# Kernel tuning notes

Measured on AMD Instinct MI355X. Metric: run time of the kernel, lower is better.

## Reference

```python
import jax, jax.numpy as jnp
import numpy as np

B, S, D, H = 4, 2048, 1024, 16
DH = D // H


def _rope_tables():
    # standard RoPE angle tables, shaped [1, S, 1, DH] as the module expects
    inv_freq = 1.0 / (10000.0 ** (np.arange(0, DH, 2, dtype=np.float32) / DH))
    ang = np.arange(S, dtype=np.float32)[:, None] * inv_freq[None, :]  # [S, DH/2]
    ang = np.concatenate([ang, ang], axis=-1)  # [S, DH]
    cos = jnp.asarray(np.cos(ang))[None, :, None, :]
    sin = jnp.asarray(np.sin(ang))[None, :, None, :]
    return cos, sin


def setup_inputs() -> dict:
    key = jax.random.key(0)
    ks = jax.random.split(key, 5)
    x = jax.random.normal(ks[0], (B, S, D), dtype=jnp.float32)
    wq = jax.random.normal(ks[1], (D, D), dtype=jnp.float32) * 0.02
    wk = jax.random.normal(ks[2], (D, D), dtype=jnp.float32) * 0.02
    wv = jax.random.normal(ks[3], (D, D), dtype=jnp.float32) * 0.02
    wo = jax.random.normal(ks[4], (D, D), dtype=jnp.float32) * 0.02
    cos, sin = _rope_tables()
    return {"x": x, "cos": cos, "sin": sin, "wq": wq, "wk": wk, "wv": wv, "wo": wo}


def _rotate_half(t):
    t1, t2 = t[..., : DH // 2], t[..., DH // 2:]
    return jnp.concatenate([-t2, t1], axis=-1)


def reference(x, cos, sin, wq, wk, wv, wo):
    b, s, d = x.shape
    # QKV projections (torch Linear: y = x @ W.T), reshape to [B, H, S, DH]
    q = (x @ wq.T).reshape(b, s, H, DH).transpose(0, 2, 1, 3)
    k = (x @ wk.T).reshape(b, s, H, DH).transpose(0, 2, 1, 3)
    v = (x @ wv.T).reshape(b, s, H, DH).transpose(0, 2, 1, 3)
    # permute(0,2,1,3): [1,S,1,DH] -> [1,1,S,DH]; slice [:, :s] is a no-op on the size-1 head dim
    cos_p = jnp.transpose(cos, (0, 2, 1, 3))[:, :s]
    sin_p = jnp.transpose(sin, (0, 2, 1, 3))[:, :s]
    q = q * cos_p + _rotate_half(q) * sin_p
    k = k * cos_p + _rotate_half(k) * sin_p
    # SDPA (no mask, dropout_p = 0)
    scores = jnp.einsum("bhqd,bhkd->bhqk", q, k) / jnp.sqrt(jnp.float32(DH))
    attn = jax.nn.softmax(scores, axis=-1)
    out = jnp.einsum("bhqk,bhkd->bhqd", attn, v)
    out = out.transpose(0, 2, 1, 3).reshape(b, s, d)
    return out @ wo.T
```

## Files before the change

kernel.cpp:

```cpp
#include <hip/hip_runtime.h>
#include <hip/hip_bf16.h>
#include <stdint.h>

#define B 4
#define S 2048
#define D 1024
#define H 16
#define DH 64
#define M_TOT (B*S)
#define BH (B*H)

typedef unsigned short u16;
typedef unsigned int u32;
typedef __attribute__((ext_vector_type(4))) float f32x4;
typedef __attribute__((ext_vector_type(16))) float f32x16;
typedef __attribute__((ext_vector_type(8))) short bf16x8;
typedef __attribute__((ext_vector_type(2))) unsigned int u32x2;

typedef const __attribute__((address_space(1))) unsigned int* gp_t;
typedef __attribute__((address_space(3))) unsigned int* lp_t;

__device__ __forceinline__ void gload_lds16(const void* g, void* l) {
    __builtin_amdgcn_global_load_lds((gp_t)g, (lp_t)l, 16, 0, 0);
}

__device__ __forceinline__ float bf2f(u16 u) {
    u32 t = ((u32)u) << 16;
    float f; __builtin_memcpy(&f, &t, 4); return f;
}
__device__ __forceinline__ u16 f2bf(float f) {
    u32 u; __builtin_memcpy(&u, &f, 4);
    u += 0x7fffu + ((u >> 16) & 1u);
    return (u16)(u >> 16);
}
__device__ __forceinline__ u32 packbf(float lo, float hi_) {
    __hip_bfloat162 h = __float22bfloat162_rn(float2{lo, hi_});
    u32 r; __builtin_memcpy(&r, &h, 4); return r;
}

__device__ __forceinline__ float exp2_fast(float x) { return __builtin_amdgcn_exp2f(x); }

#if __has_builtin(__builtin_amdgcn_permlane32_swap)
__device__ __forceinline__ void plswap(u32& a, u32& bb) {
    u32x2 r = __builtin_amdgcn_permlane32_swap(a, bb, false, false);
    a = r.x; bb = r.y;
}
#else
__device__ __forceinline__ void plswap(u32& a, u32& bb) {
    int hi = (threadIdx.x >> 5) & 1;
    u32 ra = (u32)__shfl_xor((int)a, 32);
    u32 rb = (u32)__shfl_xor((int)bb, 32);
    u32 na = hi ? rb : a;
    u32 nb = hi ? bb : ra;
    a = na; bb = nb;
}
#endif

__global__ __launch_bounds__(256)
void cvt_all_kernel(const float* __restrict__ x,
                    const float* __restrict__ wq, const float* __restrict__ wk,
                    const float* __restrict__ wv, const float* __restrict__ wo,
                    u16* __restrict__ xb, u16* __restrict__ wqb, u16* __restrict__ wkb,
                    u16* __restrict__ wvb, u16* __restrict__ wob)
{
    const size_t MD = (size_t)M_TOT * D;
    const size_t WD = (size_t)D * D;
    size_t i = ((size_t)blockIdx.x * 256 + threadIdx.x) * 8;
    const float* src; u16* dst; size_t off;
    if (i < MD) { src = x; dst = xb; off = i; }
    else {
        size_t j = i - MD;
        int wsel = (int)(j >> 20);
        off = j & (WD - 1);
        if      (wsel == 0) { src = wq; dst = wqb; }
        else if (wsel == 1) { src = wk; dst = wkb; }
        else if (wsel == 2) { src = wv; dst = wvb; }
        else                { src = wo; dst = wob; }
    }
    float4 a = *(const float4*)(src + off);
    float4 b = *(const float4*)(src + off + 4);
    union { u16 u[8]; bf16x8 v; } o;
    o.u[0] = f2bf(a.x); o.u[1] = f2bf(a.y); o.u[2] = f2bf(a.z); o.u[3] = f2bf(a.w);
    o.u[4] = f2bf(b.x); o.u[5] = f2bf(b.y); o.u[6] = f2bf(b.z); o.u[7] = f2bf(b.w);
    *(bf16x8*)(dst + off) = o.v;
}

template<int WRITE_BF16, int DO_ROPE>
__global__ __launch_bounds__(256)
void gemm_mfma(const u16* __restrict__ X,
               const u16* __restrict__ W0, const u16* __restrict__ W1, const u16* __restrict__ W2,
               void* Y0, void* Y1, void* Y2,
               const float* __restrict__ cosT, const float* __restrict__ sinT)
{
    __shared__ __align__(16) u16 Al[128 * 32];
    __shared__ __align__(16) u16 Bl[128 * 32];

    const u16* Wm = (blockIdx.z == 0) ? W0 : (blockIdx.z == 1) ? W1 : W2;
    void* Yv      = (blockIdx.z == 0) ? Y0 : (blockIdx.z == 1) ? Y1 : Y2;

    const int t = threadIdx.x;
    const int w = t >> 6, ll = t & 63;
    const int wr = w >> 1, wc = w & 1;
    const int g = ll >> 4, lc = ll & 15;
    const int m0 = blockIdx.x * 128, n0 = blockIdx.y * 128;

    const int srow = t >> 2;
    const int scol = (t & 3) * 8;

    const u16* Xa = X + (size_t)m0 * D;
    const u16* Wa = Wm + (size_t)n0 * D;

    f32x4 acc[4][4];
    #pragma unroll
    for (int i = 0; i < 4; ++i)
        #pragma unroll
        for (int j = 0; j < 4; ++j)
            acc[i][j] = (f32x4){0.f, 0.f, 0.f, 0.f};

    for (int k0 = 0; k0 < D; k0 += 32) {
        gload_lds16(Xa + (size_t)(srow)      * D + k0 + scol, &Al[(w * 64) * 8]);
        gload_lds16(Xa + (size_t)(64 + srow) * D + k0 + scol, &Al[(256 + w * 64) * 8]);
        gload_lds16(Wa + (size_t)(srow)      * D + k0 + scol, &Bl[(w * 64) * 8]);
        gload_lds16(Wa + (size_t)(64 + srow) * D + k0 + scol, &Bl[(256 + w * 64) * 8]);
        __syncthreads();

        bf16x8 af[4], bf[4];
        #pragma unroll
        for (int i = 0; i < 4; ++i)
            af[i] = *(const bf16x8*)&Al[(wr * 64 + i * 16 + lc) * 32 + g * 8];
        #pragma unroll
        for (int j = 0; j < 4; ++j)
            bf[j] = *(const bf16x8*)&Bl[(wc * 64 + j * 16 + lc) * 32 + g * 8];

        #pragma unroll
        for (int i = 0; i < 4; ++i)
            #pragma unroll
            for (int j = 0; j < 4; ++j)
                acc[i][j] = __builtin_amdgcn_mfma_f32_16x16x32_bf16(af[i], bf[j], acc[i][j], 0, 0, 0);
        __syncthreads();
    }

    if (DO_ROPE && blockIdx.z < 2) {
        const float scale = (blockIdx.z == 0) ? (0.125f * 1.44269504f) : 1.0f;
        u16* Y = (u16*)Yv;
        #pragma unroll
        for (int i = 0; i < 4; ++i)
            #pragma unroll
            for (int r = 0; r < 4; ++r) {
                int row = m0 + wr * 64 + i * 16 + g * 4 + r;
                int s = row & (S - 1);
                #pragma unroll
                for (int jh = 0; jh < 2; ++jh) {
                    float c  = cosT[s * DH + jh * 16 + lc];
                    float sn = sinT[s * DH + jh * 16 + lc];
                    float a0 = acc[i][jh][r], a1 = acc[i][jh + 2][r];
                    size_t base = (size_t)row * D + n0 + wc * 64;
                    Y[base + jh * 16 + lc]       = f2bf((a0 * c - a1 * sn) * scale);
                    Y[base + (jh + 2) * 16 + lc] = f2bf((a1 * c + a0 * sn) * scale);
                }
            }
    } else if (DO_ROPE) {
        u16* Y = (u16*)Yv;
        #pragma unroll
        for (int i = 0; i < 4; ++i)
            #pragma unroll
            for (int j = 0; j < 4; ++j) {
                int row = m0 + wr * 64 + i * 16 + g * 4;
                int col = n0 + wc * 64 + j * 16 + lc;
                int bt = row >> 11, s = row & (S - 1);
                size_t vtrow = (size_t)(bt * 16 + (col >> 6)) * 64 + (col & 63);
                u32 w0 = packbf(acc[i][j][0], acc[i][j][1]);
                u32 w1 = packbf(acc[i][j][2], acc[i][j][3]);
                u32x2 pr; pr.x = w0; pr.y = w1;
                *(u32x2*)&Y[vtrow * S + s] = pr;
            }
    } else if (WRITE_BF16) {
        u16* Y = (u16*)Yv;
        #pragma unroll
        for (int i = 0; i < 4; ++i)
            #pragma unroll
            for (int j = 0; j < 4; ++j)
                #pragma unroll
                for (int r = 0; r < 4; ++r) {
                    int row = m0 + wr * 64 + i * 16 + g * 4 + r;
                    int col = n0 + wc * 64 + j * 16 + lc;
                    Y[(size_t)row * D + col] = f2bf(acc[i][j][r]);
                }
    } else {
        float* Y = (float*)Yv;
        #pragma unroll
        for (int i = 0; i < 4; ++i)
            #pragma unroll
            for (int j = 0; j < 4; ++j)
                #pragma unroll
                for (int r = 0; r < 4; ++r) {
                    int row = m0 + wr * 64 + i * 16 + g * 4 + r;
                    int col = n0 + wc * 64 + j * 16 + lc;
                    Y[(size_t)row * D + col] = acc[i][j][r];
                }
    }
}

#define QBLK 256
#define KVT 128
#define NT (S / KVT)

__global__ __launch_bounds__(256, 2)
void attn_mfma(const u16* __restrict__ Q, const u16* __restrict__ Kg,
               const u16* __restrict__ Vt, u16* __restrict__ CTX)
{
    __shared__ __align__(16) u16 smem[32768];

    const int t  = threadIdx.x;
    const int w  = t >> 6;
    const int q  = t & 31;
    const int hi = (t >> 5) & 1;

    const int bid  = blockIdx.x;
    const int xcd  = bid & 7;
    const int slot = bid >> 3;
    const int bh   = xcd * 8 + (slot >> 3);
    const int qb   = slot & 7;
    const int b = bh >> 4, h = bh & 15;
    const int q0 = qb * QBLK;
    const int qbase = q0 + w * 64;

    bf16x8 qf[2][4];
    #pragma unroll
    for (int qg = 0; qg < 2; ++qg) {
        const u16* qp = &Q[(size_t)(b*S + qbase + qg*32 + q) * D + h*DH + hi*8];
        qf[qg][0] = *(const bf16x8*)(qp);
        qf[qg][1] = *(const bf16x8*)(qp + 16);
        qf[qg][2] = *(const bf16x8*)(qp + 32);
        qf[qg][3] = *(const bf16x8*)(qp + 48);
    }

    bf16x8 ones;
    {
        union { u16 u[8]; bf16x8 v; } ou;
        #pragma unroll
        for (int i = 0; i < 8; ++i) ou.u[i] = 0x3f80;
        ones = ou.v;
    }

    f32x16 po[4], lsum[2], zv;
    #pragma unroll
    for (int i = 0; i < 16; ++i) {
        po[0][i] = 0.f; po[1][i] = 0.f; po[2][i] = 0.f; po[3][i] = 0.f;
        lsum[0][i] = 0.f; lsum[1][i] = 0.f; zv[i] = 0.f;
    }

    const int ksrow = t >> 3;
    const int kscol = (((t & 7) << 4) ^ ((ksrow & 7) << 4)) >> 1;
    const int vsrow = t >> 4;
    const int vscol = (((t & 15) ^ (vsrow & 15)) << 3);
    const int rsw  = (q & 7) << 4;
    const int vsw  = (q & 15) << 4;

    u16* buf0 = smem;
    u16* buf1 = smem + 16384;

    const u16* kg = Kg + ((size_t)(b * S) + ksrow) * D + (size_t)h * DH + kscol;
    const u16* vg = Vt + ((size_t)bh * DH + vsrow) * S + vscol;

    #define STAGE(dst) do {                                         \
        gload_lds16(kg,           (dst) + 0*2048 + w*512);          \
        gload_lds16(kg + 32*D,    (dst) + 1*2048 + w*512);          \
        gload_lds16(kg + 64*D,    (dst) + 2*2048 + w*512);          \
        gload_lds16(kg + 96*D,    (dst) + 3*2048 + w*512);          \
        gload_lds16(vg,           (dst) + 8192 + 0*2048 + w*512);   \
        gload_lds16(vg + 16*S,    (dst) + 8192 + 1*2048 + w*512);   \
        gload_lds16(vg + 32*S,    (dst) + 8192 + 2*2048 + w*512);   \
        gload_lds16(vg + 48*S,    (dst) + 8192 + 3*2048 + w*512);   \
        kg += (size_t)KVT * D; vg += KVT; } while (0)

    auto compute = [&](const u16* base) {
        const u16* Kl = base;
        const u16* Vl = base + 8192;
        #pragma unroll
        for (int c = 0; c < 4; ++c) {
            f32x16 p0, p1;
            {
                const u16* kr = &Kl[(c*32 + q) << 6];
                bf16x8 k0 = *(const bf16x8*)&kr[((0*32 + hi*16) ^ rsw) >> 1];
                __builtin_amdgcn_s_setprio(1);
                p0 = __builtin_amdgcn_mfma_f32_32x32x16_bf16(k0, qf[0][0], zv, 0, 0, 0);
                p1 = __builtin_amdgcn_mfma_f32_32x32x16_bf16(k0, qf[1][0], zv, 0, 0, 0);
                #pragma unroll
                for (int cc = 1; cc < 4; ++cc) {
                    bf16x8 kf = *(const bf16x8*)&kr[((cc*32 + hi*16) ^ rsw) >> 1];
                    p0 = __builtin_amdgcn_mfma_f32_32x32x16_bf16(kf, qf[0][cc], p0, 0, 0, 0);
                    p1 = __builtin_amdgcn_mfma_f32_32x32x16_bf16(kf, qf[1][cc], p1, 0, 0, 0);
                }
                __builtin_amdgcn_s_setprio(0);
            }

            u32 W0[8], W1[8];
            #pragma unroll
            for (int j = 0; j < 8; ++j) {
                W0[j] = packbf(exp2_fast(p0[2*j]), exp2_fast(p0[2*j + 1]));
                W1[j] = packbf(exp2_fast(p1[2*j]), exp2_fast(p1[2*j + 1]));
            }
            plswap(W0[0], W0[2]); plswap(W0[1], W0[3]);
            plswap(W0[4], W0[6]); plswap(W0[5], W0[7]);
            plswap(W1[0], W1[2]); plswap(W1[1], W1[3]);
            plswap(W1[4], W1[6]); plswap(W1[5], W1[7]);
            bf16x8 pa0a, pa0b, pa1a, pa1b;
            {
                union { u32 u[4]; bf16x8 v; } pb;
                pb.u[0]=W0[0]; pb.u[1]=W0[1]; pb.u[2]=W0[2]; pb.u[3]=W0[3]; pa0a = pb.v;
                pb.u[0]=W0[4]; pb.u[1]=W0[5]; pb.u[2]=W0[6]; pb.u[3]=W0[7]; pa0b = pb.v;
                pb.u[0]=W1[0]; pb.u[1]=W1[1]; pb.u[2]=W1[2]; pb.u[3]=W1[3]; pa1a = pb.v;
                pb.u[0]=W1[4]; pb.u[1]=W1[5]; pb.u[2]=W1[6]; pb.u[3]=W1[7]; pa1b = pb.v;
            }

            __builtin_amdgcn_s_setprio(1);
            lsum[0] = __builtin_amdgcn_mfma_f32_32x32x16_bf16(ones, pa0a, lsum[0], 0, 0, 0);
            lsum[1] = __builtin_amdgcn_mfma_f32_32x32x16_bf16(ones, pa1a, lsum[1], 0, 0, 0);
            lsum[0] = __builtin_amdgcn_mfma_f32_32x32x16_bf16(ones, pa0b, lsum[0], 0, 0, 0);
            lsum[1] = __builtin_amdgcn_mfma_f32_32x32x16_bf16(ones, pa1b, lsum[1], 0, 0, 0);
            #pragma unroll
            for (int kk = 0; kk < 2; ++kk) {
                int vb = ((c*64 + kk*32 + hi*16) ^ vsw) >> 1;
                bf16x8 v0 = *(const bf16x8*)&Vl[(q << 7) + vb];
                bf16x8 v1 = *(const bf16x8*)&Vl[((32 + q) << 7) + vb];
                bf16x8 pq0 = kk ? pa0b : pa0a;
                bf16x8 pq1 = kk ? pa1b : pa1a;
                po[0] = __builtin_amdgcn_mfma_f32_32x32x16_bf16(v0, pq0, po[0], 0, 0, 0);
                po[1] = __builtin_amdgcn_mfma_f32_32x32x16_bf16(v1, pq0, po[1], 0, 0, 0);
                po[2] = __builtin_amdgcn_mfma_f32_32x32x16_bf16(v0, pq1, po[2], 0, 0, 0);
                po[3] = __builtin_amdgcn_mfma_f32_32x32x16_bf16(v1, pq1, po[3], 0, 0, 0);
            }
            __builtin_amdgcn_s_setprio(0);
        }
    };

    STAGE(buf0);
    asm volatile("s_waitcnt vmcnt(0)" ::: "memory");
    __builtin_amdgcn_s_barrier();

    for (int ti = 0; ti < NT; ti += 2) {
        STAGE(buf1);
        compute(buf0);
        asm volatile("s_waitcnt vmcnt(0)" ::: "memory");
        __builtin_amdgcn_s_barrier();
        if (ti < NT - 2) STAGE(buf0);
        compute(buf1);
        asm volatile("s_waitcnt vmcnt(0)" ::: "memory");
        __builtin_amdgcn_s_barrier();
    }
    #undef STAGE

    u16* ow = &smem[w * 2304];
    #pragma unroll
    for (int qg = 0; qg < 2; ++qg) {
        float inv = 1.f / lsum[qg][0];
        #pragma unroll
        for (int r = 0; r < 16; ++r) {
            int d0 = (r & 3) + 8 * (r >> 2) + 4 * hi;
            ow[q * 72 + d0]      = f2bf(po[qg*2 + 0][r] * inv);
            ow[q * 72 + 32 + d0] = f2bf(po[qg*2 + 1][r] * inv);
        }
        int row = (t & 63) >> 1, half = t & 1;
        const u16* orow = &ow[row * 72 + half * 32];
        u16* gp = &CTX[(size_t)(b*S + qbase + qg*32 + row) * D + h*DH + half * 32];
        #pragma unroll
        for (int i = 0; i < 4; ++i)
            *(bf16x8*)(gp + i * 8) = *(const bf16x8*)(orow + i * 8);
    }
}

extern "C" void kernel_launch(void* const* d_in, const int* in_sizes, int n_in,
                              void* d_out, int out_size, void* d_ws, size_t ws_size,
                              hipStream_t stream)
{
    const float* x    = (const float*)d_in[0];
    const float* cosT = (const float*)d_in[1];
    const float* sinT = (const float*)d_in[2];
    const float* wq   = (const float*)d_in[3];
    const float* wk   = (const float*)d_in[4];
    const float* wv   = (const float*)d_in[5];
    const float* wo   = (const float*)d_in[6];
    float* out = (float*)d_out;

    const size_t MD = (size_t)M_TOT * D;
    const size_t WD = (size_t)D * D;

    u16* xb   = (u16*)d_ws;
    u16* Qb   = xb + MD;
    u16* Kb   = Qb + MD;
    u16* Vtb  = Kb + MD;
    u16* CTXb = Vtb + MD;
    u16* wqb  = CTXb + MD;
    u16* wkb  = wqb + WD;
    u16* wvb  = wkb + WD;
    u16* wob  = wvb + WD;

    cvt_all_kernel<<<(int)((MD + 4*WD) / 8 / 256), 256, 0, stream>>>(
        x, wq, wk, wv, wo, xb, wqb, wkb, wvb, wob);

    gemm_mfma<1, 1><<<dim3(M_TOT / 128, D / 128, 3), 256, 0, stream>>>(
        xb, wqb, wkb, wvb, Qb, Kb, Vtb, cosT, sinT);

    attn_mfma<<<dim3(M_TOT / QBLK * H), 256, 0, stream>>>(Qb, Kb, Vtb, CTXb);

    gemm_mfma<0, 0><<<dim3(M_TOT / 128, D / 128, 1), 256, 0, stream>>>(
        CTXb, wob, nullptr, nullptr, out, nullptr, nullptr, nullptr, nullptr);
}
```

Baseline: 185.6 us.

## Add 256x256 QKV GEMM with 4-stage LDS pipeline and swizzled layout

Replaces the 128x128 QKV projection GEMM with a dedicated 256x256-tile kernel of 512 threads. It uses a 4-stage global-to-LDS ring buffer with explicit vmcnt waits and a single barrier per k-step, plus an XOR swizzle on LDS rows to avoid bank conflicts. The goals are to hide load latency, halve the barrier count and raise operand reuse per LDS byte. In exchange the kernel uses 128 KB of LDS and many more accumulator registers, which limits occupancy to one block per CU. The grid is also smaller (32x4x3 = 384 blocks), which may cause wave-quantization imbalance.

Measured after the change: 179.5 us. 1.03x faster.

```diff
diff --git a/kernel.cpp b/kernel.cpp
--- a/kernel.cpp
+++ b/kernel.cpp
@@ -85,69 +85,121 @@
     *(bf16x8*)(dst + off) = o.v;
 }
 
-template<int WRITE_BF16, int DO_ROPE>
-__global__ __launch_bounds__(256)
-void gemm_mfma(const u16* __restrict__ X,
-               const u16* __restrict__ W0, const u16* __restrict__ W1, const u16* __restrict__ W2,
-               void* Y0, void* Y1, void* Y2,
-               const float* __restrict__ cosT, const float* __restrict__ sinT)
+#define NKT 32
+
+__global__ __launch_bounds__(512)
+void gemm256_qkv(const u16* __restrict__ X,
+                 const u16* __restrict__ W0, const u16* __restrict__ W1, const u16* __restrict__ W2,
+                 u16* __restrict__ Y0, u16* __restrict__ Y1, u16* __restrict__ Y2,
+                 const float* __restrict__ cosT, const float* __restrict__ sinT)
 {
-    __shared__ __align__(16) u16 Al[128 * 32];
-    __shared__ __align__(16) u16 Bl[128 * 32];
+    __shared__ __align__(16) u16 lds[65536];
 
     const u16* Wm = (blockIdx.z == 0) ? W0 : (blockIdx.z == 1) ? W1 : W2;
-    void* Yv      = (blockIdx.z == 0) ? Y0 : (blockIdx.z == 1) ? Y1 : Y2;
-
-    const int t = threadIdx.x;
-    const int w = t >> 6, ll = t & 63;
-    const int wr = w >> 1, wc = w & 1;
-    const int g = ll >> 4, lc = ll & 15;
-    const int m0 = blockIdx.x * 128, n0 = blockIdx.y * 128;
-
-    const int srow = t >> 2;
-    const int scol = (t & 3) * 8;
+    u16* Y        = (blockIdx.z == 0) ? Y0 : (blockIdx.z == 1) ? Y1 : Y2;
+
+    const int t  = threadIdx.x;
+    const int w  = t >> 6, ll = t & 63;
+    const int lc = ll & 15, g = ll >> 4;
+    const int wr = w >> 2, wc = w & 3;
+    const int m0 = blockIdx.x * 256, n0 = blockIdx.y * 256;
+
+    const int srow   = t >> 2;
+    const int scolsw = 8 * ((t & 3) ^ ((t >> 3) & 3));
 
     const u16* Xa = X + (size_t)m0 * D;
     const u16* Wa = Wm + (size_t)n0 * D;
 
-    f32x4 acc[4][4];
-    #pragma unroll
-    for (int i = 0; i < 4; ++i)
+    int offA[8], offB[4];
+    #pragma unroll
+    for (int i = 0; i < 8; ++i) {
+        int row = wr * 128 + i * 16 + lc;
+        offA[i] = row * 32 + ((g ^ ((row >> 1) & 3)) << 3);
+    }
+    #pragma unroll
+    for (int j = 0; j < 4; ++j) {
+        int row = wc * 64 + j * 16 + lc;
+        offB[j] = row * 32 + ((g ^ ((row >> 1) & 3)) << 3);
+    }
+
+    f32x4 acc[8][4];
+    #pragma unroll
+    for (int i = 0; i < 8; ++i)
         #pragma unroll
         for (int j = 0; j < 4; ++j)
             acc[i][j] = (f32x4){0.f, 0.f, 0.f, 0.f};
 
-    for (int k0 = 0; k0 < D; k0 += 32) {
-        gload_lds16(Xa + (size_t)(srow)      * D + k0 + scol, &Al[(w * 64) * 8]);
-        gload_lds16(Xa + (size_t)(64 + srow) * D + k0 + scol, &Al[(256 + w * 64) * 8]);
-        gload_lds16(Wa + (size_t)(srow)      * D + k0 + scol, &Bl[(w * 64) * 8]);
-        gload_lds16(Wa + (size_t)(64 + srow) * D + k0 + scol, &Bl[(256 + w * 64) * 8]);
-        __syncthreads();
-
-        bf16x8 af[4], bf[4];
-        #pragma unroll
-        for (int i = 0; i < 4; ++i)
-            af[i] = *(const bf16x8*)&Al[(wr * 64 + i * 16 + lc) * 32 + g * 8];
+    #pragma unroll
+    for (int kt = 0; kt < 3; ++kt) {
+        const u16* xs = Xa + (size_t)srow * D + kt * 32 + scolsw;
+        gload_lds16(xs,           &lds[kt * 16384 + w * 512]);
+        gload_lds16(xs + 128 * D, &lds[kt * 16384 + 4096 + w * 512]);
+        const u16* ws = Wa + (size_t)srow * D + kt * 32 + scolsw;
+        gload_lds16(ws,           &lds[kt * 16384 + 8192 + w * 512]);
+        gload_lds16(ws + 128 * D, &lds[kt * 16384 + 8192 + 4096 + w * 512]);
+    }
+    asm volatile("s_waitcnt vmcnt(8)" ::: "memory");
+    __builtin_amdgcn_s_barrier();
+
+    auto body = [&](int kt, bool do_stage) {
+        const int s = kt & 3;
+        const u16* As = &lds[s * 16384];
+        const u16* Bs = &lds[s * 16384 + 8192];
+        const int kn = kt + 3;
+        const int sn = kn & 3;
+        if (do_stage) {
+            const u16* xs = Xa + (size_t)srow * D + kn * 32 + scolsw;
+            gload_lds16(xs,           &lds[sn * 16384 + w * 512]);
+            gload_lds16(xs + 128 * D, &lds[sn * 16384 + 4096 + w * 512]);
+        }
+        bf16x8 bfr[4];
         #pragma unroll
         for (int j = 0; j < 4; ++j)
-            bf[j] = *(const bf16x8*)&Bl[(wc * 64 + j * 16 + lc) * 32 + g * 8];
-
+            bfr[j] = *(const bf16x8*)&Bs[offB[j]];
+        bf16x8 afr[4];
+        #pragma unroll
+        for (int i = 0; i < 4; ++i)
+            afr[i] = *(const bf16x8*)&As[offA[i]];
         #pragma unroll
         for (int i = 0; i < 4; ++i)
             #pragma unroll
             for (int j = 0; j < 4; ++j)
-                acc[i][j] = __builtin_amdgcn_mfma_f32_16x16x32_bf16(af[i], bf[j], acc[i][j], 0, 0, 0);
-        __syncthreads();
-    }
-
-    if (DO_ROPE && blockIdx.z < 2) {
+                acc[i][j] = __builtin_amdgcn_mfma_f32_16x16x32_bf16(afr[i], bfr[j], acc[i][j], 0, 0, 0);
+        if (do_stage) {
+            const u16* ws = Wa + (size_t)srow * D + kn * 32 + scolsw;
+            gload_lds16(ws,           &lds[sn * 16384 + 8192 + w * 512]);
+            gload_lds16(ws + 128 * D, &lds[sn * 16384 + 8192 + 4096 + w * 512]);
+        }
+        #pragma unroll
+        for (int i = 0; i < 4; ++i)
+            afr[i] = *(const bf16x8*)&As[offA[i + 4]];
+        #pragma unroll
+        for (int i = 0; i < 4; ++i)
+            #pragma unroll
+            for (int j = 0; j < 4; ++j)
+                acc[i + 4][j] = __builtin_amdgcn_mfma_f32_16x16x32_bf16(afr[i], bfr[j], acc[i + 4][j], 0, 0, 0);
+    };
+
+    for (int kt = 0; kt < NKT - 3; ++kt) {
+        body(kt, true);
+        asm volatile("s_waitcnt vmcnt(8)" ::: "memory");
+        __builtin_amdgcn_s_barrier();
+    }
+    body(NKT - 3, false);
+    asm volatile("s_waitcnt vmcnt(4)" ::: "memory");
+    __builtin_amdgcn_s_barrier();
+    body(NKT - 2, false);
+    asm volatile("s_waitcnt vmcnt(0)" ::: "memory");
+    __builtin_amdgcn_s_barrier();
+    body(NKT - 1, false);
+
+    if (blockIdx.z < 2) {
         const float scale = (blockIdx.z == 0) ? (0.125f * 1.44269504f) : 1.0f;
-        u16* Y = (u16*)Yv;
-        #pragma unroll
-        for (int i = 0; i < 4; ++i)
+        #pragma unroll
+        for (int i = 0; i < 8; ++i)
             #pragma unroll
             for (int r = 0; r < 4; ++r) {
-                int row = m0 + wr * 64 + i * 16 + g * 4 + r;
+                int row = m0 + wr * 128 + i * 16 + g * 4 + r;
                 int s = row & (S - 1);
                 #pragma unroll
                 for (int jh = 0; jh < 2; ++jh) {
@@ -159,13 +211,12 @@
                     Y[base + (jh + 2) * 16 + lc] = f2bf((a1 * c + a0 * sn) * scale);
                 }
             }
-    } else if (DO_ROPE) {
-        u16* Y = (u16*)Yv;
-        #pragma unroll
-        for (int i = 0; i < 4; ++i)
+    } else {
+        #pragma unroll
+        for (int i = 0; i < 8; ++i)
             #pragma unroll
             for (int j = 0; j < 4; ++j) {
-                int row = m0 + wr * 64 + i * 16 + g * 4;
+                int row = m0 + wr * 128 + i * 16 + g * 4;
                 int col = n0 + wc * 64 + j * 16 + lc;
                 int bt = row >> 11, s = row & (S - 1);
                 size_t vtrow = (size_t)(bt * 16 + (col >> 6)) * 64 + (col & 63);
@@ -174,7 +225,65 @@
                 u32x2 pr; pr.x = w0; pr.y = w1;
                 *(u32x2*)&Y[vtrow * S + s] = pr;
             }
-    } else if (WRITE_BF16) {
+    }
+}
+
+template<int WRITE_BF16, int DO_ROPE>
+__global__ __launch_bounds__(256)
+void gemm_mfma(const u16* __restrict__ X,
+               const u16* __restrict__ W0, const u16* __restrict__ W1, const u16* __restrict__ W2,
+               void* Y0, void* Y1, void* Y2,
+               const float* __restrict__ cosT, const float* __restrict__ sinT)
+{
+    __shared__ __align__(16) u16 Al[128 * 32];
+    __shared__ __align__(16) u16 Bl[128 * 32];
+
+    const u16* Wm = (blockIdx.z == 0) ? W0 : (blockIdx.z == 1) ? W1 : W2;
+    void* Yv      = (blockIdx.z == 0) ? Y0 : (blockIdx.z == 1) ? Y1 : Y2;
+
+    const int t = threadIdx.x;
+    const int w = t >> 6, ll = t & 63;
+    const int wr = w >> 1, wc = w & 1;
+    const int g = ll >> 4, lc = ll & 15;
+    const int m0 = blockIdx.x * 128, n0 = blockIdx.y * 128;
+
+    const int srow = t >> 2;
+    const int scol = (t & 3) * 8;
+
+    const u16* Xa = X + (size_t)m0 * D;
+    const u16* Wa = Wm + (size_t)n0 * D;
+
+    f32x4 acc[4][4];
+    #pragma unroll
+    for (int i = 0; i < 4; ++i)
+        #pragma unroll
+        for (int j = 0; j < 4; ++j)
+            acc[i][j] = (f32x4){0.f, 0.f, 0.f, 0.f};
+
+    for (int k0 = 0; k0 < D; k0 += 32) {
+        gload_lds16(Xa + (size_t)(srow)      * D + k0 + scol, &Al[(w * 64) * 8]);
+        gload_lds16(Xa + (size_t)(64 + srow) * D + k0 + scol, &Al[(256 + w * 64) * 8]);
+        gload_lds16(Wa + (size_t)(srow)      * D + k0 + scol, &Bl[(w * 64) * 8]);
+        gload_lds16(Wa + (size_t)(64 + srow) * D + k0 + scol, &Bl[(256 + w * 64) * 8]);
+        __syncthreads();
+
+        bf16x8 af[4], bf[4];
+        #pragma unroll
+        for (int i = 0; i < 4; ++i)
+            af[i] = *(const bf16x8*)&Al[(wr * 64 + i * 16 + lc) * 32 + g * 8];
+        #pragma unroll
+        for (int j = 0; j < 4; ++j)
+            bf[j] = *(const bf16x8*)&Bl[(wc * 64 + j * 16 + lc) * 32 + g * 8];
+
+        #pragma unroll
+        for (int i = 0; i < 4; ++i)
+            #pragma unroll
+            for (int j = 0; j < 4; ++j)
+                acc[i][j] = __builtin_amdgcn_mfma_f32_16x16x32_bf16(af[i], bf[j], acc[i][j], 0, 0, 0);
+        __syncthreads();
+    }
+
+    if (WRITE_BF16) {
         u16* Y = (u16*)Yv;
         #pragma unroll
         for (int i = 0; i < 4; ++i)
@@ -399,7 +508,7 @@
     cvt_all_kernel<<<(int)((MD + 4*WD) / 8 / 256), 256, 0, stream>>>(
         x, wq, wk, wv, wo, xb, wqb, wkb, wvb, wob);
 
-    gemm_mfma<1, 1><<<dim3(M_TOT / 128, D / 128, 3), 256, 0, stream>>>(
+    gemm256_qkv<<<dim3(M_TOT / 256, D / 256, 3), 512, 0, stream>>>(
         xb, wqb, wkb, wvb, Qb, Kb, Vtb, cosT, sinT);
 
     attn_mfma<<<dim3(M_TOT / QBLK * H), 256, 0, stream>>>(Qb, Kb, Vtb, CTXb);
```
